# Performance work log

Measured on AMD Instinct MI355X. Metric: run time of the kernel, lower is better.

Reference implementation:

```python
import jax, jax.numpy as jnp
import numpy as np

N_FP = 235336   # n_fingerprint
N_WORD = 7844   # n_word
D = 10          # embed / hidden dim (hard-coded in module)
K = 23          # conv kernel 2*11+1
PAD = 11
N_ATOMS = 4096
L_WORDS = 65536


def setup_inputs() -> dict:
    key = jax.random.key(0)
    ks = jax.random.split(key, 16)
    s = 0.1  # weight init scale
    return {
        "fingerprints": jax.random.randint(ks[0], (N_ATOMS,), 0, N_FP),
        # scale adjacency so x + A@hs stays O(1) over 3 layers
        "adjacency": jax.random.uniform(ks[1], (N_ATOMS, N_ATOMS), dtype=jnp.float32) * (1.0 / N_ATOMS),
        "words": jax.random.randint(ks[2], (L_WORDS,), 0, N_WORD),
        "embed_fp": jax.random.normal(ks[3], (N_FP, D), dtype=jnp.float32) * s,
        "embed_word": jax.random.normal(ks[4], (N_WORD, D), dtype=jnp.float32) * s,
        "W_gnn_w": jax.random.normal(ks[5], (3, D, D), dtype=jnp.float32) * s,
        "W_gnn_b": jax.random.normal(ks[6], (3, D), dtype=jnp.float32) * s,
        "W_cnn_w": jax.random.normal(ks[7], (3, 1, 1, K, K), dtype=jnp.float32) * (s / K),
        "W_cnn_b": jax.random.normal(ks[8], (3,), dtype=jnp.float32) * s,
        "W_att_w": jax.random.normal(ks[9], (D, D), dtype=jnp.float32) * s,
        "W_att_b": jax.random.normal(ks[10], (D,), dtype=jnp.float32) * s,
        "W_out_w": jax.random.normal(ks[11], (3, 2 * D, 2 * D), dtype=jnp.float32) * s,
        "W_out_b": jax.random.normal(ks[12], (3, 2 * D), dtype=jnp.float32) * s,
        "W_int_w": jax.random.normal(ks[13], (2, 2 * D), dtype=jnp.float32) * s,
        "W_int_b": jax.random.normal(ks[14], (2,), dtype=jnp.float32) * s,
    }


def reference(fingerprints, adjacency, words, embed_fp, embed_word,
              W_gnn_w, W_gnn_b, W_cnn_w, W_cnn_b, W_att_w, W_att_b,
              W_out_w, W_out_b, W_int_w, W_int_b):
    # ---- Compound vector with GNN ----
    xs = embed_fp[fingerprints]                       # [N, D]
    for i in range(3):                                # fixed 3 layers
        hs = jax.nn.relu(xs @ W_gnn_w[i].T + W_gnn_b[i])
        xs = xs + adjacency @ hs                      # dense message passing
    compound = jnp.mean(xs, axis=0, keepdims=True)    # [1, D]

    # ---- Protein vector with attention-CNN ----
    ws = embed_word[words]                            # [L, D]
    t = ws[None, None]                                # [1,1,L,D] NCHW
    for i in range(3):
        t = jax.nn.relu(
            jax.lax.conv_general_dilated(t, W_cnn_w[i], (1, 1),
                                          [(PAD, PAD), (PAD, PAD)])
            + W_cnn_b[i])
    xs_p = t[0, 0]                                    # [L, D]

    h = jax.nn.relu(compound @ W_att_w.T + W_att_b)   # [1, D]
    hs_p = jax.nn.relu(xs_p @ W_att_w.T + W_att_b)    # [L, D]
    weights = jnp.tanh(h @ hs_p.T)                    # [1, L]
    ys = weights.T * hs_p                             # [L, D]
    protein = jnp.mean(ys, axis=0, keepdims=True)     # [1, D]

    # ---- Fusion MLP ----
    cat = jnp.concatenate([compound, protein], axis=1)  # [1, 2D]
    for j in range(3):
        cat = jax.nn.relu(cat @ W_out_w[j].T + W_out_b[j])
    return cat @ W_int_w.T + W_int_b                  # [1, 2]
```

## Files before the change

kernel.cpp:

```cpp
#include <hip/hip_runtime.h>
#include <hip/hip_bf16.h>
#include <math.h>

#define N_ATOMS 4096
#define L_WORDS 65536
#define DD 10
#define HALO 11

#define CONV_BLOCKS 256
#define CONV_BLOCK 256
#define GNN_BLOCKS 512
#define RPW 8
#define RPB 32
#define QCOLS 1024

__global__ __launch_bounds__(256) void gnn_embed(
    const int* __restrict__ fp, const float* __restrict__ embed_fp,
    float* __restrict__ xs0)
{
    int n = blockIdx.x * blockDim.x + threadIdx.x;
    if (n >= N_ATOMS) return;
    const float* e = embed_fp + (size_t)fp[n] * DD;
    #pragma unroll
    for (int d = 0; d < DD; ++d) xs0[n * DD + d] = e[d];
}

__global__ __launch_bounds__(256, 3) void fused_layer(
    const float* __restrict__ A,
    const float* __restrict__ xs0,
    const float* __restrict__ p0,
    const float* __restrict__ p1,
    float* __restrict__ part,
    const float* __restrict__ Wg, const float* __restrict__ bg,
    const float* __restrict__ tin, const int* __restrict__ words,
    const float* __restrict__ embed_word, const float* __restrict__ w,
    const float* __restrict__ bptr, float* __restrict__ tout)
{
    __shared__ float sh[DD * QCOLS];
    const int tid = threadIdx.x;

    if (blockIdx.x < CONV_BLOCKS) {
        float* s = sh;
        const int l0 = blockIdx.x * CONV_BLOCK;
        for (int idx = tid; idx < (CONV_BLOCK + 2 * HALO) * DD; idx += CONV_BLOCK) {
            int rr = idx / DD, d = idx - rr * DD;
            int gr = l0 - HALO + rr;
            float v = 0.f;
            if (gr >= 0 && gr < L_WORDS) {
                if (tin) v = tin[(size_t)gr * DD + d];
                else     v = embed_word[(size_t)words[gr] * DD + d];
            }
            s[rr * 11 + d] = v;
        }
        __syncthreads();

        const float bias = *bptr;
        float acc[DD];
        #pragma unroll
        for (int d = 0; d < DD; ++d) acc[d] = bias;
        for (int i = 0; i < 23; ++i) {
            float row[DD];
            const float* sr = &s[(tid + i) * 11];
            #pragma unroll
            for (int c = 0; c < DD; ++c) row[c] = sr[c];
            #pragma unroll
            for (int d = 0; d < DD; ++d) {
                #pragma unroll
                for (int c = 0; c < DD; ++c)
                    acc[d] += row[c] * w[i * 23 + (c - d + 11)];
            }
        }
        const int l = l0 + tid;
        #pragma unroll
        for (int d = 0; d < DD; ++d)
            tout[(size_t)l * DD + d] = fmaxf(acc[d], 0.f);
    } else {
        const int b = blockIdx.x - CONV_BLOCKS;
        const int wave = tid >> 6, lane = tid & 63;
        const int q = b & 3, rg = b >> 2;
        const int qbase = q * QCOLS;

        for (int j = 0; j < 4; ++j) {
            const int lc = j * 256 + tid;
            const int n = qbase + lc;
            float x[DD];
            #pragma unroll
            for (int d = 0; d < DD; ++d) x[d] = xs0[n * DD + d];
            if (p0) {
                #pragma unroll
                for (int qq = 0; qq < 4; ++qq)
                    #pragma unroll
                    for (int d = 0; d < DD; ++d)
                        x[d] += p0[((size_t)qq * N_ATOMS + n) * DD + d];
            }
            if (p1) {
                #pragma unroll
                for (int qq = 0; qq < 4; ++qq)
                    #pragma unroll
                    for (int d = 0; d < DD; ++d)
                        x[d] += p1[((size_t)qq * N_ATOMS + n) * DD + d];
            }
            #pragma unroll
            for (int d = 0; d < DD; ++d) {
                float v = bg[d];
                #pragma unroll
                for (int k = 0; k < DD; ++k) v += Wg[d * DD + k] * x[k];
                sh[d * QCOLS + lc] = fmaxf(v, 0.f);
            }
        }
        __syncthreads();

        const int r0 = rg * RPB + wave * RPW;
        const float4* A4 = (const float4*)(A + (size_t)r0 * N_ATOMS) + q * (QCOLS / 4);
        const float4* sh4 = (const float4*)sh;

        float acc[RPW][DD];
        #pragma unroll
        for (int r = 0; r < RPW; ++r)
            #pragma unroll
            for (int d = 0; d < DD; ++d) acc[r][d] = 0.f;

        #pragma unroll 1
        for (int it = 0; it < 4; ++it) {
            const int cb = it * 64 + lane;
            float4 a[RPW];
            #pragma unroll
            for (int r = 0; r < RPW; ++r) a[r] = A4[r * (N_ATOMS / 4) + cb];
            #pragma unroll
            for (int d = 0; d < DD; ++d) {
                float4 h = sh4[d * 256 + cb];
                #pragma unroll
                for (int r = 0; r < RPW; ++r) {
                    acc[r][d] += a[r].x * h.x;
                    acc[r][d] += a[r].y * h.y;
                    acc[r][d] += a[r].z * h.z;
                    acc[r][d] += a[r].w * h.w;
                }
            }
        }

        #pragma unroll
        for (int m = 1; m <= 4; m <<= 1) {
            #pragma unroll
            for (int r = 0; r < RPW; ++r)
                #pragma unroll
                for (int d = 0; d < DD; ++d)
                    acc[r][d] += __shfl_xor(acc[r][d], m, 64);
        }
        __syncthreads();

        if ((lane & 7) == 0) {
            const int g = lane >> 3;
            float* dst = &sh[(wave * 8 + g) * 80];
            #pragma unroll
            for (int r = 0; r < RPW; ++r)
                #pragma unroll
                for (int d = 0; d < DD; ++d) dst[r * DD + d] = acc[r][d];
        }
        __syncthreads();

        float* pdst = part + ((size_t)q * N_ATOMS + rg * RPB) * DD;
        for (int o = tid; o < RPB * DD; o += 256) {
            const int w8 = o / 80;
            const int k = o - w8 * 80;
            float v = 0.f;
            #pragma unroll
            for (int g = 0; g < 8; ++g) v += sh[(w8 * 8 + g) * 80 + k];
            pdst[o] = v;
        }
    }
}

__global__ __launch_bounds__(256) void comp_reduce(
    const float* __restrict__ xs0, const float* __restrict__ p0,
    const float* __restrict__ p1, const float* __restrict__ p2,
    float* __restrict__ comp_part)
{
    const int tid = threadIdx.x, wave = tid >> 6, lane = tid & 63;
    const int n = blockIdx.x * 256 + tid;
    float x[DD];
    #pragma unroll
    for (int d = 0; d < DD; ++d) {
        float v = xs0[n * DD + d];
        #pragma unroll
        for (int qq = 0; qq < 4; ++qq) {
            v += p0[((size_t)qq * N_ATOMS + n) * DD + d];
            v += p1[((size_t)qq * N_ATOMS + n) * DD + d];
            v += p2[((size_t)qq * N_ATOMS + n) * DD + d];
        }
        x[d] = v;
    }
    #pragma unroll
    for (int m = 32; m >= 1; m >>= 1) {
        #pragma unroll
        for (int d = 0; d < DD; ++d) x[d] += __shfl_xor(x[d], m, 64);
    }
    __shared__ float s[4][DD];
    if (lane == 0) {
        #pragma unroll
        for (int d = 0; d < DD; ++d) s[wave][d] = x[d];
    }
    __syncthreads();
    if (tid < DD)
        comp_part[blockIdx.x * DD + tid] =
            s[0][tid] + s[1][tid] + s[2][tid] + s[3][tid];
}

__global__ __launch_bounds__(1024) void attention_pool(
    const float* __restrict__ xs_p, const float* __restrict__ comp_part,
    const float* __restrict__ Wa, const float* __restrict__ ba,
    float* __restrict__ att_part)
{
    __shared__ float shc[DD];
    __shared__ float s[16][DD];
    const int tid = threadIdx.x, wave = tid >> 6, lane = tid & 63;
    const int l = blockIdx.x * 1024 + tid;

    if (tid < DD) {
        float c = 0.f;
        #pragma unroll
        for (int p = 0; p < 16; ++p) c += comp_part[p * DD + tid];
        shc[tid] = c * (1.f / N_ATOMS);
    }
    __syncthreads();

    float h[DD];
    #pragma unroll
    for (int d = 0; d < DD; ++d) {
        float v = ba[d];
        #pragma unroll
        for (int k = 0; k < DD; ++k) v += Wa[d * DD + k] * shc[k];
        h[d] = fmaxf(v, 0.f);
    }

    float row[DD];
    #pragma unroll
    for (int d = 0; d < DD; ++d) row[d] = xs_p[(size_t)l * DD + d];

    float hp[DD], dotv = 0.f;
    #pragma unroll
    for (int d = 0; d < DD; ++d) {
        float v = ba[d];
        #pragma unroll
        for (int k = 0; k < DD; ++k) v += Wa[d * DD + k] * row[k];
        hp[d] = fmaxf(v, 0.f);
        dotv += h[d] * hp[d];
    }
    const float wgt = tanhf(dotv);

    float y[DD];
    #pragma unroll
    for (int d = 0; d < DD; ++d) y[d] = wgt * hp[d];
    #pragma unroll
    for (int m = 32; m >= 1; m >>= 1) {
        #pragma unroll
        for (int d = 0; d < DD; ++d) y[d] += __shfl_xor(y[d], m, 64);
    }
    if (lane == 0) {
        #pragma unroll
        for (int d = 0; d < DD; ++d) s[wave][d] = y[d];
    }
    __syncthreads();
    if (tid < DD) {
        float v = 0.f;
        #pragma unroll
        for (int wv = 0; wv < 16; ++wv) v += s[wv][tid];
        att_part[blockIdx.x * DD + tid] = v;
    }
}

__global__ __launch_bounds__(64) void final_mlp(
    const float* __restrict__ comp_part, const float* __restrict__ att_part,
    const float* __restrict__ Wo, const float* __restrict__ bo,
    const float* __restrict__ Wi, const float* __restrict__ bi,
    float* __restrict__ out)
{
    const int t = threadIdx.x;
    float a[DD];
    #pragma unroll
    for (int d = 0; d < DD; ++d) a[d] = att_part[t * DD + d];
    #pragma unroll
    for (int m = 32; m >= 1; m >>= 1) {
        #pragma unroll
        for (int d = 0; d < DD; ++d) a[d] += __shfl_xor(a[d], m, 64);
    }
    __shared__ float cat[20];
    if (t < DD) {
        float c = 0.f;
        #pragma unroll
        for (int p = 0; p < 16; ++p) c += comp_part[p * DD + t];
        cat[t] = c * (1.f / N_ATOMS);
    }
    if (t == 0) {
        #pragma unroll
        for (int d = 0; d < DD; ++d) cat[DD + d] = a[d] * (1.f / L_WORDS);
    }
    __syncthreads();
    for (int j = 0; j < 3; ++j) {
        float v = 0.f;
        if (t < 20) {
            v = bo[j * 20 + t];
            for (int k = 0; k < 20; ++k) v += Wo[j * 400 + t * 20 + k] * cat[k];
        }
        __syncthreads();
        if (t < 20) cat[t] = fmaxf(v, 0.f);
        __syncthreads();
    }
    if (t < 2) {
        float v = bi[t];
        for (int k = 0; k < 20; ++k) v += Wi[t * 20 + k] * cat[k];
        out[t] = v;
    }
}

extern "C" void kernel_launch(void* const* d_in, const int* in_sizes, int n_in,
                              void* d_out, int out_size, void* d_ws, size_t ws_size,
                              hipStream_t stream)
{
    const int*   fp     = (const int*)d_in[0];
    const float* A      = (const float*)d_in[1];
    const int*   words  = (const int*)d_in[2];
    const float* emb_fp = (const float*)d_in[3];
    const float* emb_w  = (const float*)d_in[4];
    const float* Wg     = (const float*)d_in[5];
    const float* bg     = (const float*)d_in[6];
    const float* Wc     = (const float*)d_in[7];
    const float* bc     = (const float*)d_in[8];
    const float* Wa     = (const float*)d_in[9];
    const float* ba     = (const float*)d_in[10];
    const float* Wo     = (const float*)d_in[11];
    const float* bo     = (const float*)d_in[12];
    const float* Wi     = (const float*)d_in[13];
    const float* bi     = (const float*)d_in[14];
    float* out = (float*)d_out;
    float* ws  = (float*)d_ws;

    float* xs0   = ws;
    float* ta    = ws + 40960;
    float* tb    = ws + 696320;
    float* part0 = ws + 1351680;
    float* part1 = ws + 1515520;
    float* part2 = ws + 1679360;
    float* comp_part = ws + 1843200;
    float* att_part  = ws + 1843456;

    const int fused_grid = CONV_BLOCKS + GNN_BLOCKS;

    gnn_embed<<<N_ATOMS / 256, 256, 0, stream>>>(fp, emb_fp, xs0);

    fused_layer<<<fused_grid, 256, 0, stream>>>(
        A, xs0, nullptr, nullptr, part0, Wg, bg,
        nullptr, words, emb_w, Wc, bc, ta);

    fused_layer<<<fused_grid, 256, 0, stream>>>(
        A, xs0, part0, nullptr, part1, Wg + 100, bg + 10,
        ta, nullptr, nullptr, Wc + 529, bc + 1, tb);

    fused_layer<<<fused_grid, 256, 0, stream>>>(
        A, xs0, part0, part1, part2, Wg + 200, bg + 20,
        tb, nullptr, nullptr, Wc + 1058, bc + 2, ta);

    comp_reduce<<<16, 256, 0, stream>>>(xs0, part0, part1, part2, comp_part);

    attention_pool<<<L_WORDS / 1024, 1024, 0, stream>>>(
        ta, comp_part, Wa, ba, att_part);

    final_mlp<<<1, 64, 0, stream>>>(comp_part, att_part, Wo, bo, Wi, bi, out);
}
```

Before: 204.3 us.

## Fold embedding gather into layers, interleave partials, use nontemporal A loads

```diff
diff --git a/kernel.cpp b/kernel.cpp
--- a/kernel.cpp
+++ b/kernel.cpp
@@ -14,20 +14,13 @@
 #define RPB 32
 #define QCOLS 1024
 
-__global__ __launch_bounds__(256) void gnn_embed(
-    const int* __restrict__ fp, const float* __restrict__ embed_fp,
-    float* __restrict__ xs0)
-{
-    int n = blockIdx.x * blockDim.x + threadIdx.x;
-    if (n >= N_ATOMS) return;
-    const float* e = embed_fp + (size_t)fp[n] * DD;
-    #pragma unroll
-    for (int d = 0; d < DD; ++d) xs0[n * DD + d] = e[d];
-}
+typedef float v4f __attribute__((ext_vector_type(4)));
+
 
 __global__ __launch_bounds__(256, 3) void fused_layer(
     const float* __restrict__ A,
-    const float* __restrict__ xs0,
+    const int* __restrict__ fp,
+    const float* __restrict__ embed_fp,
     const float* __restrict__ p0,
     const float* __restrict__ p1,
     float* __restrict__ part,
@@ -84,21 +77,22 @@
             const int lc = j * 256 + tid;
             const int n = qbase + lc;
             float x[DD];
-            #pragma unroll
-            for (int d = 0; d < DD; ++d) x[d] = xs0[n * DD + d];
+            const float* e = embed_fp + (size_t)fp[n] * DD;
+            #pragma unroll
+            for (int d = 0; d < DD; ++d) x[d] = e[d];
             if (p0) {
+                const float* pp = p0 + (size_t)n * 40;
                 #pragma unroll
                 for (int qq = 0; qq < 4; ++qq)
                     #pragma unroll
-                    for (int d = 0; d < DD; ++d)
-                        x[d] += p0[((size_t)qq * N_ATOMS + n) * DD + d];
+                    for (int d = 0; d < DD; ++d) x[d] += pp[qq * 10 + d];
             }
             if (p1) {
+                const float* pp = p1 + (size_t)n * 40;
                 #pragma unroll
                 for (int qq = 0; qq < 4; ++qq)
                     #pragma unroll
-                    for (int d = 0; d < DD; ++d)
-                        x[d] += p1[((size_t)qq * N_ATOMS + n) * DD + d];
+                    for (int d = 0; d < DD; ++d) x[d] += pp[qq * 10 + d];
             }
             #pragma unroll
             for (int d = 0; d < DD; ++d) {
@@ -111,8 +105,8 @@
         __syncthreads();
 
         const int r0 = rg * RPB + wave * RPW;
-        const float4* A4 = (const float4*)(A + (size_t)r0 * N_ATOMS) + q * (QCOLS / 4);
-        const float4* sh4 = (const float4*)sh;
+        const v4f* A4 = (const v4f*)(A + (size_t)r0 * N_ATOMS) + q * (QCOLS / 4);
+        const v4f* sh4 = (const v4f*)sh;
 
         float acc[RPW][DD];
         #pragma unroll
@@ -123,18 +117,25 @@
         #pragma unroll 1
         for (int it = 0; it < 4; ++it) {
             const int cb = it * 64 + lane;
-            float4 a[RPW];
-            #pragma unroll
-            for (int r = 0; r < RPW; ++r) a[r] = A4[r * (N_ATOMS / 4) + cb];
-            #pragma unroll
-            for (int d = 0; d < DD; ++d) {
-                float4 h = sh4[d * 256 + cb];
-                #pragma unroll
-                for (int r = 0; r < RPW; ++r) {
-                    acc[r][d] += a[r].x * h.x;
-                    acc[r][d] += a[r].y * h.y;
-                    acc[r][d] += a[r].z * h.z;
-                    acc[r][d] += a[r].w * h.w;
+            v4f h4[DD];
+            #pragma unroll
+            for (int d = 0; d < DD; ++d) h4[d] = sh4[d * 256 + cb];
+            #pragma unroll
+            for (int rb = 0; rb < RPW; rb += 4) {
+                v4f a[4];
+                #pragma unroll
+                for (int r = 0; r < 4; ++r)
+                    a[r] = __builtin_nontemporal_load(
+                        &A4[(size_t)(rb + r) * (N_ATOMS / 4) + cb]);
+                #pragma unroll
+                for (int r = 0; r < 4; ++r) {
+                    #pragma unroll
+                    for (int d = 0; d < DD; ++d) {
+                        acc[rb + r][d] += a[r].x * h4[d].x;
+                        acc[rb + r][d] += a[r].y * h4[d].y;
+                        acc[rb + r][d] += a[r].z * h4[d].z;
+                        acc[rb + r][d] += a[r].w * h4[d].w;
+                    }
                 }
             }
         }
@@ -159,37 +160,39 @@
         }
         __syncthreads();
 
-        float* pdst = part + ((size_t)q * N_ATOMS + rg * RPB) * DD;
+        float* pbase = part + (size_t)rg * (RPB * 40) + q * 10;
         for (int o = tid; o < RPB * DD; o += 256) {
             const int w8 = o / 80;
             const int k = o - w8 * 80;
             float v = 0.f;
             #pragma unroll
             for (int g = 0; g < 8; ++g) v += sh[(w8 * 8 + g) * 80 + k];
-            pdst[o] = v;
+            const int row = w8 * 8 + k / 10;
+            const int d = k % 10;
+            pbase[row * 40 + d] = v;
         }
     }
 }
 
 __global__ __launch_bounds__(256) void comp_reduce(
-    const float* __restrict__ xs0, const float* __restrict__ p0,
-    const float* __restrict__ p1, const float* __restrict__ p2,
-    float* __restrict__ comp_part)
+    const int* __restrict__ fp, const float* __restrict__ embed_fp,
+    const float* __restrict__ p0, const float* __restrict__ p1,
+    const float* __restrict__ p2, float* __restrict__ comp_part)
 {
     const int tid = threadIdx.x, wave = tid >> 6, lane = tid & 63;
     const int n = blockIdx.x * 256 + tid;
     float x[DD];
-    #pragma unroll
-    for (int d = 0; d < DD; ++d) {
-        float v = xs0[n * DD + d];
-        #pragma unroll
-        for (int qq = 0; qq < 4; ++qq) {
-            v += p0[((size_t)qq * N_ATOMS + n) * DD + d];
-            v += p1[((size_t)qq * N_ATOMS + n) * DD + d];
-            v += p2[((size_t)qq * N_ATOMS + n) * DD + d];
-        }
-        x[d] = v;
-    }
+    const float* e = embed_fp + (size_t)fp[n] * DD;
+    #pragma unroll
+    for (int d = 0; d < DD; ++d) x[d] = e[d];
+    const float* a0 = p0 + (size_t)n * 40;
+    const float* a1 = p1 + (size_t)n * 40;
+    const float* a2 = p2 + (size_t)n * 40;
+    #pragma unroll
+    for (int qq = 0; qq < 4; ++qq)
+        #pragma unroll
+        for (int d = 0; d < DD; ++d)
+            x[d] += a0[qq * 10 + d] + a1[qq * 10 + d] + a2[qq * 10 + d];
     #pragma unroll
     for (int m = 32; m >= 1; m >>= 1) {
         #pragma unroll
@@ -335,32 +338,29 @@
     float* out = (float*)d_out;
     float* ws  = (float*)d_ws;
 
-    float* xs0   = ws;
-    float* ta    = ws + 40960;
-    float* tb    = ws + 696320;
-    float* part0 = ws + 1351680;
-    float* part1 = ws + 1515520;
-    float* part2 = ws + 1679360;
-    float* comp_part = ws + 1843200;
-    float* att_part  = ws + 1843456;
+    float* ta    = ws;
+    float* tb    = ws + 655360;
+    float* part0 = ws + 1310720;
+    float* part1 = ws + 1474560;
+    float* part2 = ws + 1638400;
+    float* comp_part = ws + 1802240;
+    float* att_part  = ws + 1802496;
 
     const int fused_grid = CONV_BLOCKS + GNN_BLOCKS;
 
-    gnn_embed<<<N_ATOMS / 256, 256, 0, stream>>>(fp, emb_fp, xs0);
-
     fused_layer<<<fused_grid, 256, 0, stream>>>(
-        A, xs0, nullptr, nullptr, part0, Wg, bg,
+        A, fp, emb_fp, nullptr, nullptr, part0, Wg, bg,
         nullptr, words, emb_w, Wc, bc, ta);
 
     fused_layer<<<fused_grid, 256, 0, stream>>>(
-        A, xs0, part0, nullptr, part1, Wg + 100, bg + 10,
+        A, fp, emb_fp, part0, nullptr, part1, Wg + 100, bg + 10,
         ta, nullptr, nullptr, Wc + 529, bc + 1, tb);
 
     fused_layer<<<fused_grid, 256, 0, stream>>>(
-        A, xs0, part0, part1, part2, Wg + 200, bg + 20,
+        A, fp, emb_fp, part0, part1, part2, Wg + 200, bg + 20,
         tb, nullptr, nullptr, Wc + 1058, bc + 2, ta);
 
-    comp_reduce<<<16, 256, 0, stream>>>(xs0, part0, part1, part2, comp_part);
+    comp_reduce<<<16, 256, 0, stream>>>(fp, emb_fp, part0, part1, part2, comp_part);
 
     attention_pool<<<L_WORDS / 1024, 1024, 0, stream>>>(
         ta, comp_part, Wa, ba, att_part);
```

New measurement: 218.3 us. +6.8%, slower.
